# Performance work log

Measured on AMD Instinct MI355X. Metric: run time of the kernel, lower is better.

Reference implementation:

```python
import jax, jax.numpy as jnp
import numpy as np


def setup_inputs() -> dict:
    key = jax.random.key(0)
    k1, k2, k3 = jax.random.split(key, 3)
    N, E, D_IN, D_OUT = 100000, 1600000, 64, 64
    x = jax.random.normal(k1, (N, D_IN), dtype=jnp.float32)
    edge_index = jax.random.randint(k2, (2, E), 0, N, dtype=jnp.int64)
    # Glorot-style init for the GCN weight, zero bias (PyG defaults)
    W = jax.random.normal(k3, (D_IN, D_OUT), dtype=jnp.float32) * (1.0 / np.sqrt(D_IN))
    b = jnp.zeros((D_OUT,), dtype=jnp.float32)
    return {"x": x, "edge_index": edge_index, "W": W, "b": b}


def reference(x, edge_index, W, b):
    # GCNConv (PyG semantics, add_self_loops=True, normalize=True) followed by
    # Dropout (eval mode -> identity) and ReLU.
    N = x.shape[0]
    # Linear transform first (small GEMM)
    xw = x @ W  # [N, D_OUT]
    # Add self-loops
    loops = jnp.arange(N, dtype=edge_index.dtype)
    row = jnp.concatenate([edge_index[0], loops])  # source nodes
    col = jnp.concatenate([edge_index[1], loops])  # destination nodes
    # Symmetric degree normalization: deg over destination index (PyG gcn_norm)
    ones = jnp.ones(col.shape[0], dtype=xw.dtype)
    deg = jax.ops.segment_sum(ones, col, num_segments=N)
    deg_inv_sqrt = jnp.where(deg > 0, jax.lax.rsqrt(deg), 0.0)
    norm = deg_inv_sqrt[row] * deg_inv_sqrt[col]  # [E+N]
    # Gather source features, scale, scatter-add to destinations
    msgs = norm[:, None] * xw[row]  # [E+N, D_OUT]
    out = jax.ops.segment_sum(msgs, col, num_segments=N)
    out = out + b
    # dropout in eval mode is identity
    return jax.nn.relu(out)
```

## Files before the change

kernel.cpp:

```cpp
#include <hip/hip_runtime.h>
#include <hip/hip_fp16.h>


#define D 64
#define BW 256
#define CAP 6144
#define EPT 16
#define PART_T 256
#define EPB (PART_T * EPT)

__global__ void k_part(const int* __restrict__ row, const int* __restrict__ col,
                       int* __restrict__ gcur, int* __restrict__ packed,
                       int E, int NBUCK) {
    extern __shared__ int sh[];
    int* lh   = sh;
    int* base = sh + NBUCK;
    for (int i = threadIdx.x; i < NBUCK; i += PART_T) lh[i] = 0;
    __syncthreads();
    int e0 = blockIdx.x * EPB + threadIdx.x;
    int rr[EPT], cc[EPT], pp[EPT];
#pragma unroll
    for (int i = 0; i < EPT; ++i) {
        int e = e0 + i * PART_T;
        if (e < E) {
            cc[i] = col[e];
            rr[i] = row[e];
            pp[i] = atomicAdd(&lh[cc[i] >> 8], 1);
        } else {
            cc[i] = -1;
        }
    }
    __syncthreads();
    int rot = (int)((blockIdx.x * 97u) % (unsigned)NBUCK);
    for (int j = threadIdx.x; j < NBUCK; j += PART_T) {
        int bu = j + rot; if (bu >= NBUCK) bu -= NBUCK;
        int h = lh[bu];
        if (h > 0) base[bu] = atomicAdd(&gcur[bu * 32], h);
    }
    __syncthreads();
#pragma unroll
    for (int i = 0; i < EPT; ++i) {
        if (cc[i] >= 0) {
            int bu = cc[i] >> 8;
            int pos = base[bu] + pp[i];
            if (pos < CAP)
                packed[(size_t)bu * CAP + pos] = (rr[i] << 8) | (cc[i] & 255);
        }
    }
}

__global__ void k_dis(const int* __restrict__ gcur, const int* __restrict__ packed,
                      float* __restrict__ dis, int N) {
    __shared__ int lh[BW];
    int b = blockIdx.x;
    lh[threadIdx.x] = 0;
    __syncthreads();
    int sz = min(gcur[b * 32], CAP);
    const int* pk = packed + (size_t)b * CAP;
    for (int i = threadIdx.x; i < sz; i += BW)
        atomicAdd(&lh[pk[i] & 255], 1);
    __syncthreads();
    int n = b * BW + threadIdx.x;
    if (n < N) dis[n] = rsqrtf((float)(lh[threadIdx.x] + 1));
}

__global__ void k_gemm_scale(const float* __restrict__ x, const float* __restrict__ W,
                             const float* __restrict__ dis, __half2* __restrict__ xw_h,
                             int N) {
    __shared__ float Ws[D][D];
    __shared__ float xs[8][D];
    int tx = threadIdx.x & 31;
    int ty = threadIdx.x >> 5;
    for (int i = threadIdx.x; i < D * D; i += 256) Ws[i >> 6][i & 63] = W[i];
    for (int i = threadIdx.x; i < 8 * D; i += 256) {
        int rr = blockIdx.x * 8 + (i >> 6);
        xs[i >> 6][i & 63] = (rr < N) ? x[(size_t)rr * D + (i & 63)] : 0.f;
    }
    __syncthreads();
    int row = blockIdx.x * 8 + ty;
    if (row < N) {
        float a0 = 0.f, a1 = 0.f;
#pragma unroll
        for (int k = 0; k < D; ++k) {
            float xv = xs[ty][k];
            a0 = fmaf(xv, Ws[k][2 * tx + 0], a0);
            a1 = fmaf(xv, Ws[k][2 * tx + 1], a1);
        }
        float w = dis[row];
        xw_h[(size_t)row * 32 + tx] = __floats2half2_rn(a0 * w, a1 * w);
    }
}

__global__ __launch_bounds__(1024, 8)
void k_gather(const int* __restrict__ gcur, const int* __restrict__ packed,
              const uint2* __restrict__ xwh, const float* __restrict__ bias,
              float4* __restrict__ out4, int N) {
    __shared__ int lh[BW], stt[BW], cur[BW];
    __shared__ int srtL[CAP];
    __shared__ int wsum[4];
    int b = blockIdx.x;
    int tid = threadIdx.x;
    if (tid < BW) lh[tid] = 0;
    __syncthreads();
    int sz = min(gcur[b * 32], CAP);
    const int* pk = packed + (size_t)b * CAP;
    for (int i = tid; i < sz; i += 1024)
        atomicAdd(&lh[pk[i] & 255], 1);
    __syncthreads();
    int lane = tid & 63, wv4 = tid >> 6;
    int v = (tid < BW) ? lh[tid] : 0;
    int s = v;
#pragma unroll
    for (int off = 1; off < 64; off <<= 1) {
        int u = __shfl_up(s, off);
        if (lane >= off) s += u;
    }
    if (tid < BW && lane == 63) wsum[wv4] = s;
    __syncthreads();
    if (tid < BW) {
        int woff = 0;
        for (int w = 0; w < 4; ++w) woff += (w < wv4) ? wsum[w] : 0;
        int st = woff + s - v;
        stt[tid] = st;
        cur[tid] = st;
    }
    __syncthreads();
    for (int i = tid; i < sz; i += 1024) {
        int p = pk[i];
        int pos = atomicAdd(&cur[p & 255], 1);
        srtL[pos] = p >> 8;
    }
    __syncthreads();
    int wv = tid >> 6;
    int q = lane >> 4;
    int l = lane & 15;
    const float4 bb = ((const float4*)bias)[l];
#define ADDV(h)                                                     \
    {                                                               \
        __half2 h0 = *(__half2*)&(h).x, h1 = *(__half2*)&(h).y;     \
        float2 f0 = __half22float2(h0), f1 = __half22float2(h1);    \
        acc.x += f0.x; acc.y += f0.y; acc.z += f1.x; acc.w += f1.y; \
    }
    for (int nn = wv * 16; nn < wv * 16 + 16; ++nn) {
        int node = b * BW + nn;
        if (node >= N) break;
        int k = lh[nn], s0 = stt[nn];
        float4 acc = make_float4(0.f, 0.f, 0.f, 0.f);
        if (q == 0) { uint2 hs = xwh[(size_t)node * 16 + l]; ADDV(hs); }
        int j = q;
        for (; j + 4 < k; j += 8) {
            int r0 = srtL[s0 + j];
            int r1 = srtL[s0 + j + 4];
            uint2 va = xwh[(size_t)r0 * 16 + l];
            uint2 vb = xwh[(size_t)r1 * 16 + l];
            ADDV(va); ADDV(vb);
        }
        if (j < k) { uint2 vc = xwh[(size_t)srtL[s0 + j] * 16 + l]; ADDV(vc); }
#pragma unroll
        for (int m = 16; m < 64; m <<= 1) {
            acc.x += __shfl_xor(acc.x, m);
            acc.y += __shfl_xor(acc.y, m);
            acc.z += __shfl_xor(acc.z, m);
            acc.w += __shfl_xor(acc.w, m);
        }
        if (q == 0) {
            float dn = rsqrtf((float)(k + 1));
            float4 o;
            o.x = fmaxf(fmaf(dn, acc.x, bb.x), 0.f);
            o.y = fmaxf(fmaf(dn, acc.y, bb.y), 0.f);
            o.z = fmaxf(fmaf(dn, acc.z, bb.z), 0.f);
            o.w = fmaxf(fmaf(dn, acc.w, bb.w), 0.f);
            out4[(size_t)node * 16 + l] = o;
        }
    }
#undef ADDV
}

extern "C" void kernel_launch(void* const* d_in, const int* in_sizes, int n_in,
                              void* d_out, int out_size, void* d_ws, size_t ws_size,
                              hipStream_t stream) {
    const float* x    = (const float*)d_in[0];
    const int*   ei   = (const int*)d_in[1];
    const float* W    = (const float*)d_in[2];
    const float* bias = (const float*)d_in[3];
    float* out = (float*)d_out;

    const int N = in_sizes[0] / D;
    const int E = in_sizes[1] / 2;
    const int* row = ei;
    const int* col = ei + E;

    const int NBUCK = (N + BW - 1) / BW;
    const int NB1   = (E + EPB - 1) / EPB;

    char* ws = (char*)d_ws;
    size_t off = 0;
    __half2* xw_h = (__half2*)(ws + off); off += (size_t)N * 32 * sizeof(__half2);
    int* packed   = (int*)(ws + off);     off += (size_t)NBUCK * CAP * sizeof(int);
    int* gcur     = (int*)(ws + off);     off += (size_t)NBUCK * 32 * sizeof(int);
    float* dis    = (float*)(ws + off);   off += (size_t)N * sizeof(float);

    size_t ldsPart = 2u * (size_t)NBUCK * sizeof(int);

    hipMemsetAsync(gcur, 0, (size_t)NBUCK * 32 * sizeof(int), stream);
    k_part<<<NB1, PART_T, ldsPart, stream>>>(row, col, gcur, packed, E, NBUCK);
    k_dis<<<NBUCK, BW, 0, stream>>>(gcur, packed, dis, N);
    k_gemm_scale<<<(N + 7) / 8, 256, 0, stream>>>(x, W, dis, xw_h, N);
    k_gather<<<NBUCK, 1024, 0, stream>>>(gcur, packed, (const uint2*)xw_h, bias,
                                         (float4*)out, N);
}
```

Before: 189.1 us.

## Use bf16 MFMA for the feature GEMM and unroll the gather loop four-way

Replaces the scalar FMA GEMM with a bf16 MFMA (16x16x32) kernel that converts x and W to bf16 in registers, computes 16-row tiles per wave, and writes the dis-scaled result as fp16. The gather loop now issues four independent row loads per iteration instead of two, which raises memory-level parallelism for the random neighbor reads. Converting inputs to bf16 adds rounding error in xw. The output stores are scattered 2-byte writes, so they may coalesce poorly.

```diff
diff --git a/kernel.cpp b/kernel.cpp
--- a/kernel.cpp
+++ b/kernel.cpp
@@ -8,6 +8,15 @@
 #define EPT 16
 #define PART_T 256
 #define EPB (PART_T * EPT)
+
+typedef __attribute__((ext_vector_type(8))) short bf16x8;
+typedef __attribute__((ext_vector_type(4))) float f32x4;
+
+__device__ __forceinline__ unsigned short f2bf(float f) {
+    unsigned u = __float_as_uint(f);
+    u += 0x7FFFu + ((u >> 16) & 1u);
+    return (unsigned short)(u >> 16);
+}
 
 __global__ void k_part(const int* __restrict__ row, const int* __restrict__ col,
                        int* __restrict__ gcur, int* __restrict__ packed,
@@ -64,31 +73,62 @@
     if (n < N) dis[n] = rsqrtf((float)(lh[threadIdx.x] + 1));
 }
 
-__global__ void k_gemm_scale(const float* __restrict__ x, const float* __restrict__ W,
-                             const float* __restrict__ dis, __half2* __restrict__ xw_h,
-                             int N) {
-    __shared__ float Ws[D][D];
-    __shared__ float xs[8][D];
-    int tx = threadIdx.x & 31;
-    int ty = threadIdx.x >> 5;
-    for (int i = threadIdx.x; i < D * D; i += 256) Ws[i >> 6][i & 63] = W[i];
-    for (int i = threadIdx.x; i < 8 * D; i += 256) {
-        int rr = blockIdx.x * 8 + (i >> 6);
-        xs[i >> 6][i & 63] = (rr < N) ? x[(size_t)rr * D + (i & 63)] : 0.f;
-    }
-    __syncthreads();
-    int row = blockIdx.x * 8 + ty;
-    if (row < N) {
-        float a0 = 0.f, a1 = 0.f;
-#pragma unroll
-        for (int k = 0; k < D; ++k) {
-            float xv = xs[ty][k];
-            a0 = fmaf(xv, Ws[k][2 * tx + 0], a0);
-            a1 = fmaf(xv, Ws[k][2 * tx + 1], a1);
-        }
-        float w = dis[row];
-        xw_h[(size_t)row * 32 + tx] = __floats2half2_rn(a0 * w, a1 * w);
-    }
+__global__ __launch_bounds__(256, 4)
+void k_gemm_mfma(const float* __restrict__ x, const float* __restrict__ W,
+                 const float* __restrict__ dis, unsigned short* __restrict__ xw_h,
+                 int N) {
+    __shared__ float Ws[64 * 64];
+    int tid = threadIdx.x;
+    for (int i = tid; i < 4096; i += 256) Ws[i] = W[i];
+    __syncthreads();
+    int lane = tid & 63, wv = tid >> 6;
+    int m = lane & 15, quad = lane >> 4;
+    bf16x8 Bf[4][2];
+#pragma unroll
+    for (int t = 0; t < 4; ++t)
+#pragma unroll
+        for (int s = 0; s < 2; ++s) {
+            bf16x8 f;
+#pragma unroll
+            for (int j = 0; j < 8; ++j)
+                f[j] = (short)f2bf(Ws[(s * 32 + quad * 8 + j) * 64 + t * 16 + m]);
+            Bf[t][s] = f;
+        }
+    int mt = blockIdx.x * 4 + wv;
+    int row0 = mt * 16;
+    if (row0 >= N) return;
+    const float* xr = x + (size_t)(row0 + m) * 64 + quad * 8;
+    float4 a0 = *(const float4*)(xr);
+    float4 a1 = *(const float4*)(xr + 4);
+    float4 a2 = *(const float4*)(xr + 32);
+    float4 a3 = *(const float4*)(xr + 36);
+    bf16x8 A0, A1;
+    A0[0] = (short)f2bf(a0.x); A0[1] = (short)f2bf(a0.y);
+    A0[2] = (short)f2bf(a0.z); A0[3] = (short)f2bf(a0.w);
+    A0[4] = (short)f2bf(a1.x); A0[5] = (short)f2bf(a1.y);
+    A0[6] = (short)f2bf(a1.z); A0[7] = (short)f2bf(a1.w);
+    A1[0] = (short)f2bf(a2.x); A1[1] = (short)f2bf(a2.y);
+    A1[2] = (short)f2bf(a2.z); A1[3] = (short)f2bf(a2.w);
+    A1[4] = (short)f2bf(a3.x); A1[5] = (short)f2bf(a3.y);
+    A1[6] = (short)f2bf(a3.z); A1[7] = (short)f2bf(a3.w);
+    f32x4 acc[4];
+#pragma unroll
+    for (int t = 0; t < 4; ++t) {
+        acc[t] = (f32x4){0.f, 0.f, 0.f, 0.f};
+        acc[t] = __builtin_amdgcn_mfma_f32_16x16x32_bf16(A0, Bf[t][0], acc[t], 0, 0, 0);
+        acc[t] = __builtin_amdgcn_mfma_f32_16x16x32_bf16(A1, Bf[t][1], acc[t], 0, 0, 0);
+    }
+    float4 dv = *(const float4*)(dis + row0 + quad * 4);
+    float dsc[4] = {dv.x, dv.y, dv.z, dv.w};
+#pragma unroll
+    for (int t = 0; t < 4; ++t)
+#pragma unroll
+        for (int r = 0; r < 4; ++r) {
+            int grow = row0 + quad * 4 + r;
+            int gcol = t * 16 + m;
+            xw_h[(size_t)grow * 64 + gcol] =
+                __half_as_ushort(__float2half(acc[t][r] * dsc[r]));
+        }
 }
 
 __global__ __launch_bounds__(1024, 8)
@@ -148,20 +188,24 @@
         float4 acc = make_float4(0.f, 0.f, 0.f, 0.f);
         if (q == 0) { uint2 hs = xwh[(size_t)node * 16 + l]; ADDV(hs); }
         int j = q;
-        for (; j + 4 < k; j += 8) {
+        for (; j + 12 < k; j += 16) {
             int r0 = srtL[s0 + j];
             int r1 = srtL[s0 + j + 4];
+            int r2 = srtL[s0 + j + 8];
+            int r3 = srtL[s0 + j + 12];
             uint2 va = xwh[(size_t)r0 * 16 + l];
             uint2 vb = xwh[(size_t)r1 * 16 + l];
-            ADDV(va); ADDV(vb);
-        }
-        if (j < k) { uint2 vc = xwh[(size_t)srtL[s0 + j] * 16 + l]; ADDV(vc); }
-#pragma unroll
-        for (int m = 16; m < 64; m <<= 1) {
-            acc.x += __shfl_xor(acc.x, m);
-            acc.y += __shfl_xor(acc.y, m);
-            acc.z += __shfl_xor(acc.z, m);
-            acc.w += __shfl_xor(acc.w, m);
+            uint2 vc = xwh[(size_t)r2 * 16 + l];
+            uint2 vd = xwh[(size_t)r3 * 16 + l];
+            ADDV(va); ADDV(vb); ADDV(vc); ADDV(vd);
+        }
+        for (; j < k; j += 4) { uint2 ve = xwh[(size_t)srtL[s0 + j] * 16 + l]; ADDV(ve); }
+#pragma unroll
+        for (int mm = 16; mm < 64; mm <<= 1) {
+            acc.x += __shfl_xor(acc.x, mm);
+            acc.y += __shfl_xor(acc.y, mm);
+            acc.z += __shfl_xor(acc.z, mm);
+            acc.w += __shfl_xor(acc.w, mm);
         }
         if (q == 0) {
             float dn = rsqrtf((float)(k + 1));
@@ -192,10 +236,11 @@
 
     const int NBUCK = (N + BW - 1) / BW;
     const int NB1   = (E + EPB - 1) / EPB;
+    const int NT    = (N + 15) / 16;
 
     char* ws = (char*)d_ws;
     size_t off = 0;
-    __half2* xw_h = (__half2*)(ws + off); off += (size_t)N * 32 * sizeof(__half2);
+    unsigned short* xw_h = (unsigned short*)(ws + off); off += (size_t)N * D * sizeof(unsigned short);
     int* packed   = (int*)(ws + off);     off += (size_t)NBUCK * CAP * sizeof(int);
     int* gcur     = (int*)(ws + off);     off += (size_t)NBUCK * 32 * sizeof(int);
     float* dis    = (float*)(ws + off);   off += (size_t)N * sizeof(float);
@@ -205,7 +250,7 @@
     hipMemsetAsync(gcur, 0, (size_t)NBUCK * 32 * sizeof(int), stream);
     k_part<<<NB1, PART_T, ldsPart, stream>>>(row, col, gcur, packed, E, NBUCK);
     k_dis<<<NBUCK, BW, 0, stream>>>(gcur, packed, dis, N);
-    k_gemm_scale<<<(N + 7) / 8, 256, 0, stream>>>(x, W, dis, xw_h, N);
+    k_gemm_mfma<<<(NT + 3) / 4, 256, 0, stream>>>(x, W, dis, xw_h, N);
     k_gather<<<NBUCK, 1024, 0, stream>>>(gcur, packed, (const uint2*)xw_h, bias,
                                          (float4*)out, N);
 }
```

After: 160.9 us. -14.9%, faster.
